# Performance work log

Measured on AMD Instinct MI355X. Metric: run time of the kernel, lower is better.

Reference implementation:

```python
import jax, jax.numpy as jnp
import numpy as np

R = 2  # radius from sigma_wh == 1: int((1*6 - 1)/2) = 2 -> fixed 5x5 patch
P = 2 * R + 1

# Design matrix for log-domain Gaussian least-squares fit:
# log z = c0 + c1*x + c2*y + c3*x^2 + c4*y^2
_ys, _xs = np.meshgrid(np.arange(-R, R + 1), np.arange(-R, R + 1), indexing='ij')
_xs = _xs.reshape(-1).astype(np.float32)
_ys = _ys.reshape(-1).astype(np.float32)
_M = np.stack([np.ones_like(_xs), _xs, _ys, _xs ** 2, _ys ** 2], axis=1)  # [25,5]
PINV = jnp.asarray(np.linalg.pinv(_M))  # [5,25]


def _neg_loss(pred, gt):
    pos = (gt == 1.0).astype(pred.dtype)
    neg = (gt < 1.0).astype(pred.dtype)
    neg_w = (1.0 - gt) ** 4
    pos_loss = (jnp.log(pred) * (1.0 - pred) ** 2 * pos).sum()
    neg_loss = (jnp.log(1.0 - pred) * pred ** 2 * neg_w * neg).sum()
    num_pos = pos.sum()
    denom = jnp.where(num_pos == 0, 1.0, num_pos)
    return jnp.where(num_pos == 0, -neg_loss, -(pos_loss + neg_loss) / denom)


def setup_inputs() -> dict:
    key = jax.random.key(0)
    k1, k2, k3, k4 = jax.random.split(key, 4)
    B, C, H, W, O = 8, 80, 128, 128, 128
    return {
        'hm_out': jax.random.normal(k1, (B, C, H, W), jnp.float32),
        'hm_gt': jax.random.uniform(k2, (B, C, H, W), jnp.float32),
        'ct_ind': jax.random.randint(k3, (B, C, O, 2), 0, 124).astype(jnp.int32),
        'sigma_wh': jnp.ones((B, C, O, 2), jnp.float32),
        'hm_mask': jnp.ones((B, C, H, W), jnp.float32),
        'sigmawh_mask': jax.random.randint(k4, (B, C, O), 0, 2).astype(jnp.int32),
    }


def reference(hm_out, hm_gt, ct_ind, sigma_wh, hm_mask, sigmawh_mask):
    B, C, H, W = hm_out.shape
    O = ct_ind.shape[2]

    # --- focal loss (second call in original overwrites the first) ---
    hm_s = jax.nn.sigmoid(hm_out)
    pred = jnp.clip(hm_s, 1e-6, 1.0 - 1e-6)
    focal = _neg_loss(pred, hm_gt * hm_mask)

    # --- batched per-object 5x5 patch gather (replaces python triple loop) ---
    x = jnp.clip(ct_ind[..., 0], R, W - 1 - R)  # [B,C,O]
    y = jnp.clip(ct_ind[..., 1], R, H - 1 - R)
    off = jnp.arange(-R, R + 1)
    yy = y[..., None, None] + off[:, None]            # [B,C,O,P,1]
    xx = x[..., None, None] + off[None, :]            # [B,C,O,1,P]
    b_idx = jnp.arange(B)[:, None, None, None, None]
    c_idx = jnp.arange(C)[None, :, None, None, None]
    patch = hm_s[b_idx, c_idx, yy, xx]                # [B,C,O,P,P]
    logz = jnp.log(patch).reshape(B, C, O, P * P)

    # --- batched gaussian fit: least squares in log domain ---
    coef = jnp.einsum('bcop,kp->bcok', logz, PINV)    # [B,C,O,5]
    bx, by, ax, ay = coef[..., 1], coef[..., 2], coef[..., 3], coef[..., 4]
    ax_s = jnp.where(jnp.abs(ax) < 1e-12, -1.0, ax)
    ay_s = jnp.where(jnp.abs(ay) < 1e-12, -1.0, ay)
    sw2 = -0.5 / ax_s   # fitted variance along w
    sh2 = -0.5 / ay_s   # fitted variance along h
    mu_w = -bx / (2.0 * ax_s)
    mu_h = -by / (2.0 * ay_s)

    # original loop: obj in range(mask.sum()) and mask[obj]==1
    cnt = sigmawh_mask.sum(axis=-1)                                  # [B,C]
    in_loop = jnp.arange(O)[None, None, :] < cnt[..., None]
    valid = (sigmawh_mask == 1) & in_loop & (sw2 > 0) & (sh2 > 0)

    sgw = sigma_wh[..., 0]
    sgh = sigma_wh[..., 1]
    osw = jnp.where(valid, sw2, 1.0)
    osh = jnp.where(valid, sh2, 1.0)
    omw = jnp.where(valid, mu_w, 0.0)
    omh = jnp.where(valid, mu_h, 0.0)
    sgw2 = jnp.where(valid, sgw, 1.0) ** 2
    sgh2 = jnp.where(valid, sgh, 1.0) ** 2

    kl = (0.5 * jnp.log(sgw2 * sgh2 / (osw * osh)) - 1.0
          + 0.5 * (osw / sgw2 + osh / sgh2)
          + 0.5 * (omw ** 2 / sgw2 + omh ** 2 / sgh2))
    kl_sum = jnp.where(valid, kl, 0.0).sum()
    return (kl_sum, focal)
```

## Files before the change

kernel.cpp:

```cpp
#include <hip/hip_runtime.h>
#include <math.h>

#define Bn 8
#define Cn 80
#define Hn 128
#define Wn 128
#define On 128

#define KL_BLOCKS 320
#define FOCAL_BLOCKS 5120
#define TOTAL_BLOCKS (KL_BLOCKS + FOCAL_BLOCKS)

#define WS_LOSS 0
#define WS_NP FOCAL_BLOCKS
#define WS_KL (2 * FOCAL_BLOCKS)

__global__ __launch_bounds__(256) void fused_kernel(
    const float4* __restrict__ hm_out4, const float4* __restrict__ hm_gt4,
    const float4* __restrict__ hm_mask4, const float* __restrict__ hm_out,
    const int* __restrict__ ct_ind, const float* __restrict__ sigma_wh,
    const int* __restrict__ sigmawh_mask, double* __restrict__ ws) {
    __shared__ int si[256];
    __shared__ double sd[8];
    const int t = threadIdx.x;

    if (blockIdx.x >= KL_BLOCKS) {
        const int bid = blockIdx.x - KL_BLOCKS;
        const int base = bid * 512 + t;

        float4 xo0 = hm_out4[base];
        float4 xo1 = hm_out4[base + 256];
        float4 xg0 = hm_gt4[base];
        float4 xg1 = hm_gt4[base + 256];
        float4 xm0 = hm_mask4[base];
        float4 xm1 = hm_mask4[base + 256];

        float loss = 0.0f, np = 0.0f;
        const float* po[2] = {(const float*)&xo0, (const float*)&xo1};
        const float* pg[2] = {(const float*)&xg0, (const float*)&xg1};
        const float* pm[2] = {(const float*)&xm0, (const float*)&xm1};
#pragma unroll
        for (int it = 0; it < 2; ++it) {
#pragma unroll
            for (int k = 0; k < 4; ++k) {
                float x = po[it][k];
                float g = pg[it][k] * pm[it][k];
                float e = __expf(-x);
                float tt = 1.0f + e;
                float s = __builtin_amdgcn_rcpf(tt);
                float lt = __logf(tt);
                float ls = -lt;
                float l1s = -x - lt;

                float om = 1.0f - s;
                float pos_c = ls * om * om;
                float omg = 1.0f - g;
                float w2 = omg * omg;
                float neg_c = l1s * (s * s) * (w2 * w2);

                bool is_pos = (g == 1.0f);
                float contrib = is_pos ? pos_c : ((g < 1.0f) ? neg_c : 0.0f);
                loss += contrib;
                np += is_pos ? 1.0f : 0.0f;
            }
        }

        for (int off = 32; off > 0; off >>= 1) {
            loss += __shfl_down(loss, off, 64);
            np += __shfl_down(np, off, 64);
        }
        int wave = t >> 6, lane = t & 63;
        if (lane == 0) {
            sd[wave * 2 + 0] = (double)loss;
            sd[wave * 2 + 1] = (double)np;
        }
        __syncthreads();
        if (t == 0) {
            double L = sd[0] + sd[2] + sd[4] + sd[6];
            double N = sd[1] + sd[3] + sd[5] + sd[7];
            ws[WS_LOSS + bid] = L;
            ws[WS_NP + bid] = N;
        }
    } else {
        const int grp = t >> 7;
        const int o = t & 127;
        const int bc = blockIdx.x * 2 + grp;

        int m = sigmawh_mask[bc * On + o];
        si[t] = m;
        __syncthreads();
#pragma unroll
        for (int s = 64; s > 0; s >>= 1) {
            if ((t & 127) < s) si[t] += si[t + s];
            __syncthreads();
        }
        const int cnt = si[grp << 7];

        float kl = 0.0f;
        if (m == 1 && o < cnt) {
            int gi = (bc * On + o) * 2;
            int xi = min(max(ct_ind[gi + 0], 2), Wn - 3);
            int yi = min(max(ct_ind[gi + 1], 2), Hn - 3);
            const float* base = hm_out + ((size_t)bc * Hn + yi) * Wn + xi;

            float v[25];
#pragma unroll
            for (int py = 0; py < 5; ++py)
#pragma unroll
                for (int px = 0; px < 5; ++px)
                    v[py * 5 + px] = base[(py - 2) * Wn + (px - 2)];

            float Sbx = 0.f, Sby = 0.f, Sax = 0.f, Say = 0.f;
#pragma unroll
            for (int py = 0; py < 5; ++py) {
#pragma unroll
                for (int px = 0; px < 5; ++px) {
                    float lz = -__logf(1.0f + __expf(-v[py * 5 + px]));
                    float fx = (float)(px - 2), fy = (float)(py - 2);
                    Sbx += fx * lz;
                    Sby += fy * lz;
                    Sax += (fx * fx - 2.0f) * lz;
                    Say += (fy * fy - 2.0f) * lz;
                }
            }
            float bx = Sbx * (1.0f / 50.0f);
            float by = Sby * (1.0f / 50.0f);
            float ax = Sax * (1.0f / 70.0f);
            float ay = Say * (1.0f / 70.0f);

            float ax_s = (fabsf(ax) < 1e-12f) ? -1.0f : ax;
            float ay_s = (fabsf(ay) < 1e-12f) ? -1.0f : ay;
            float sw2 = -0.5f / ax_s;
            float sh2 = -0.5f / ay_s;

            if (sw2 > 0.0f && sh2 > 0.0f) {
                float mw = -bx / (2.0f * ax_s);
                float mh = -by / (2.0f * ay_s);
                float sgw = sigma_wh[gi + 0];
                float sgh = sigma_wh[gi + 1];
                float sgw2 = sgw * sgw;
                float sgh2 = sgh * sgh;
                kl = 0.5f * __logf(sgw2 * sgh2 / (sw2 * sh2)) - 1.0f +
                     0.5f * (sw2 / sgw2 + sh2 / sgh2) +
                     0.5f * (mw * mw / sgw2 + mh * mh / sgh2);
            }
        }

        for (int off = 32; off > 0; off >>= 1) kl += __shfl_down(kl, off, 64);
        int wave = t >> 6, lane = t & 63;
        if (lane == 0) sd[wave] = (double)kl;
        __syncthreads();
        if (t == 0) ws[WS_KL + blockIdx.x] = sd[0] + sd[1] + sd[2] + sd[3];
    }
}

__global__ __launch_bounds__(1024) void finalize_kernel(
    const double* __restrict__ ws, float* __restrict__ out) {
    int t = threadIdx.x;
    double L = 0, N = 0, K = 0;
    for (int i = t; i < FOCAL_BLOCKS; i += 1024) {
        L += ws[WS_LOSS + i];
        N += ws[WS_NP + i];
    }
    if (t < KL_BLOCKS) K = ws[WS_KL + t];

    for (int off = 32; off > 0; off >>= 1) {
        L += __shfl_down(L, off, 64);
        N += __shfl_down(N, off, 64);
        K += __shfl_down(K, off, 64);
    }
    __shared__ double sm[16 * 3];
    int wave = t >> 6, lane = t & 63;
    if (lane == 0) {
        sm[wave * 3 + 0] = L;
        sm[wave * 3 + 1] = N;
        sm[wave * 3 + 2] = K;
    }
    __syncthreads();
    if (t == 0) {
        double a = 0, c = 0, d = 0;
#pragma unroll
        for (int w = 0; w < 16; ++w) {
            a += sm[w * 3 + 0];
            c += sm[w * 3 + 1];
            d += sm[w * 3 + 2];
        }
        double denom = (c == 0.0) ? 1.0 : c;
        out[0] = (float)d;
        out[1] = (float)(-a / denom);
    }
}

extern "C" void kernel_launch(void* const* d_in, const int* in_sizes, int n_in,
                              void* d_out, int out_size, void* d_ws,
                              size_t ws_size, hipStream_t stream) {
    const float* hm_out       = (const float*)d_in[0];
    const float* hm_gt        = (const float*)d_in[1];
    const int*   ct_ind       = (const int*)d_in[2];
    const float* sigma_wh     = (const float*)d_in[3];
    const float* hm_mask      = (const float*)d_in[4];
    const int*   sigmawh_mask = (const int*)d_in[5];
    double* ws = (double*)d_ws;
    float* out = (float*)d_out;

    fused_kernel<<<TOTAL_BLOCKS, 256, 0, stream>>>(
        (const float4*)hm_out, (const float4*)hm_gt, (const float4*)hm_mask,
        hm_out, ct_ind, sigma_wh, sigmawh_mask, ws);

    finalize_kernel<<<1, 1024, 0, stream>>>(ws, out);
}
```

Measured before the change: 150.8 us.

## Make the focal loop grid-stride with prefetch and count masks via ballot

The focal-loss part now runs on a quarter as many blocks. Each thread walks 8 float4 elements at a grid stride and loads the next element's hm_out, hm_gt and hm_mask before computing on the current one, so loads overlap the transcendental math. This also cuts block scheduling overhead and the number of per-block partial sums that finalize has to add up. In the KL blocks, the shared-memory tree reduction that counts the mask (7 barriers) is replaced by a wave ballot plus popcount, which assumes the mask holds only 0 or 1.

```diff
diff --git a/kernel.cpp b/kernel.cpp
--- a/kernel.cpp
+++ b/kernel.cpp
@@ -8,7 +8,9 @@
 #define On 128
 
 #define KL_BLOCKS 320
-#define FOCAL_BLOCKS 5120
+#define FOCAL_BLOCKS 1280
+#define FOCAL_ITERS 8
+#define FOCAL_STRIDE (FOCAL_BLOCKS * 256)
 #define TOTAL_BLOCKS (KL_BLOCKS + FOCAL_BLOCKS)
 
 #define WS_LOSS 0
@@ -20,47 +22,71 @@
     const float4* __restrict__ hm_mask4, const float* __restrict__ hm_out,
     const int* __restrict__ ct_ind, const float* __restrict__ sigma_wh,
     const int* __restrict__ sigmawh_mask, double* __restrict__ ws) {
-    __shared__ int si[256];
     __shared__ double sd[8];
+    __shared__ int si[4];
     const int t = threadIdx.x;
 
     if (blockIdx.x >= KL_BLOCKS) {
         const int bid = blockIdx.x - KL_BLOCKS;
-        const int base = bid * 512 + t;
-
-        float4 xo0 = hm_out4[base];
-        float4 xo1 = hm_out4[base + 256];
-        float4 xg0 = hm_gt4[base];
-        float4 xg1 = hm_gt4[base + 256];
-        float4 xm0 = hm_mask4[base];
-        float4 xm1 = hm_mask4[base + 256];
+        int i = bid * 256 + t;
+
+        float4 a = hm_out4[i];
+        float4 g4 = hm_gt4[i];
+        float4 m4 = hm_mask4[i];
 
         float loss = 0.0f, np = 0.0f;
-        const float* po[2] = {(const float*)&xo0, (const float*)&xo1};
-        const float* pg[2] = {(const float*)&xg0, (const float*)&xg1};
-        const float* pm[2] = {(const float*)&xm0, (const float*)&xm1};
-#pragma unroll
-        for (int it = 0; it < 2; ++it) {
+
+#pragma unroll 1
+        for (int it = 0; it < FOCAL_ITERS - 1; ++it) {
+            const int j = i + FOCAL_STRIDE;
+            float4 a2 = hm_out4[j];
+            float4 g2 = hm_gt4[j];
+            float4 m2 = hm_mask4[j];
+
+            const float* po = (const float*)&a;
+            const float* pg = (const float*)&g4;
+            const float* pm = (const float*)&m4;
 #pragma unroll
             for (int k = 0; k < 4; ++k) {
-                float x = po[it][k];
-                float g = pg[it][k] * pm[it][k];
+                float x = po[k];
+                float g = pg[k] * pm[k];
                 float e = __expf(-x);
                 float tt = 1.0f + e;
                 float s = __builtin_amdgcn_rcpf(tt);
                 float lt = __logf(tt);
-                float ls = -lt;
-                float l1s = -x - lt;
-
                 float om = 1.0f - s;
-                float pos_c = ls * om * om;
+                float pos_c = -lt * om * om;
                 float omg = 1.0f - g;
                 float w2 = omg * omg;
-                float neg_c = l1s * (s * s) * (w2 * w2);
-
+                float neg_c = (-x - lt) * (s * s) * (w2 * w2);
                 bool is_pos = (g == 1.0f);
-                float contrib = is_pos ? pos_c : ((g < 1.0f) ? neg_c : 0.0f);
-                loss += contrib;
+                loss += is_pos ? pos_c : ((g < 1.0f) ? neg_c : 0.0f);
+                np += is_pos ? 1.0f : 0.0f;
+            }
+            a = a2;
+            g4 = g2;
+            m4 = m2;
+            i = j;
+        }
+        {
+            const float* po = (const float*)&a;
+            const float* pg = (const float*)&g4;
+            const float* pm = (const float*)&m4;
+#pragma unroll
+            for (int k = 0; k < 4; ++k) {
+                float x = po[k];
+                float g = pg[k] * pm[k];
+                float e = __expf(-x);
+                float tt = 1.0f + e;
+                float s = __builtin_amdgcn_rcpf(tt);
+                float lt = __logf(tt);
+                float om = 1.0f - s;
+                float pos_c = -lt * om * om;
+                float omg = 1.0f - g;
+                float w2 = omg * omg;
+                float neg_c = (-x - lt) * (s * s) * (w2 * w2);
+                bool is_pos = (g == 1.0f);
+                loss += is_pos ? pos_c : ((g < 1.0f) ? neg_c : 0.0f);
                 np += is_pos ? 1.0f : 0.0f;
             }
         }
@@ -76,25 +102,20 @@
         }
         __syncthreads();
         if (t == 0) {
-            double L = sd[0] + sd[2] + sd[4] + sd[6];
-            double N = sd[1] + sd[3] + sd[5] + sd[7];
-            ws[WS_LOSS + bid] = L;
-            ws[WS_NP + bid] = N;
+            ws[WS_LOSS + bid] = sd[0] + sd[2] + sd[4] + sd[6];
+            ws[WS_NP + bid] = sd[1] + sd[3] + sd[5] + sd[7];
         }
     } else {
         const int grp = t >> 7;
         const int o = t & 127;
         const int bc = blockIdx.x * 2 + grp;
-
-        int m = sigmawh_mask[bc * On + o];
-        si[t] = m;
+        const int wave = t >> 6, lane = t & 63;
+
+        const int m = sigmawh_mask[bc * On + o];
+        unsigned long long bal = __ballot(m == 1);
+        if (lane == 0) si[wave] = __popcll(bal);
         __syncthreads();
-#pragma unroll
-        for (int s = 64; s > 0; s >>= 1) {
-            if ((t & 127) < s) si[t] += si[t + s];
-            __syncthreads();
-        }
-        const int cnt = si[grp << 7];
+        const int cnt = si[grp * 2] + si[grp * 2 + 1];
 
         float kl = 0.0f;
         if (m == 1 && o < cnt) {
@@ -147,7 +168,6 @@
         }
 
         for (int off = 32; off > 0; off >>= 1) kl += __shfl_down(kl, off, 64);
-        int wave = t >> 6, lane = t & 63;
         if (lane == 0) sd[wave] = (double)kl;
         __syncthreads();
         if (t == 0) ws[WS_KL + blockIdx.x] = sd[0] + sd[1] + sd[2] + sd[3];
```

After: 152.6 us. No clear change (+1.2%).
